# Kernel optimization log

Measured on AMD Instinct MI355X. Metric: run time of the kernel, lower is better.

## Reference

```python
import jax, jax.numpy as jnp
import numpy as np

BETA = 0.1
NUM_LAYERS = 2  # GT layers inside each FastGTN


def densify(edge_index, edge_weight, num_nodes):
    # edge_index: [T, 2, E] int, edge_weight: [T, E] -> dense [T, N, N]
    T, _, E = edge_index.shape
    t_ids = jnp.broadcast_to(jnp.arange(T)[:, None], (T, E))
    dense = jnp.zeros((T, num_nodes, num_nodes), dtype=edge_weight.dtype)
    return dense.at[t_ids, edge_index[:, 0, :], edge_index[:, 1, :]].add(edge_weight)


def fast_gtn(dense_A, X, Ws, conv_w, lin_w, lin_b, num_nodes):
    # Ws: [C, w_in, w_out]; conv_w: [L, C, T]; lin_w: [C*w_out, w_out]
    H = jnp.einsum('nk,ckh->cnh', X, Ws)              # [C, N, w_out]
    X_ = jax.lax.stop_gradient(H)                      # clone().detach()
    for l in range(NUM_LAYERS):
        filt = jax.nn.softmax(conv_w[l], axis=1)       # [C, T]
        adj = jnp.einsum('ct,tij->cij', filt, dense_A) # [C, N, N]
        H = jnp.einsum('cij,cjh->cih', adj, H)         # graph conv per channel
    H_ = jax.nn.relu(BETA * X_ + (1.0 - BETA) * H)     # [C, N, w_out]
    H_ = jnp.transpose(H_, (1, 0, 2)).reshape(num_nodes, -1)  # [N, C*w_out]
    return jax.nn.relu(H_ @ lin_w + lin_b)             # [N, w_out]


def setup_inputs() -> dict:
    key = jax.random.key(0)
    ks = jax.random.split(key, 12)
    T, E, N = 4, 131072, 4096
    C, F_IN, H_OUT = 2, 128, 64
    edge_index = jax.random.randint(ks[0], (T, 2, E), 0, N, dtype=jnp.int64)
    edge_weight = jax.random.uniform(ks[1], (T, E), dtype=jnp.float32)
    X = jax.random.normal(ks[2], (N, F_IN), dtype=jnp.float32)
    def glorot(k, shape):
        fan_in, fan_out = shape[-2], shape[-1]
        s = jnp.sqrt(6.0 / (fan_in + fan_out))
        return jax.random.uniform(k, shape, jnp.float32, -s, s)
    # FastGTN #1 (w_in=F_IN)
    Ws1 = glorot(ks[3], (C, F_IN, H_OUT))
    conv_w1 = 0.1 * jax.random.normal(ks[4], (NUM_LAYERS, C, T), dtype=jnp.float32)
    lin_w1 = glorot(ks[5], (C * H_OUT, H_OUT))
    lin_b1 = jnp.zeros((H_OUT,), jnp.float32)
    # FastGTN #2 (w_in=H_OUT)
    Ws2 = glorot(ks[6], (C, H_OUT, H_OUT))
    conv_w2 = 0.1 * jax.random.normal(ks[7], (NUM_LAYERS, C, T), dtype=jnp.float32)
    lin_w2 = glorot(ks[8], (C * H_OUT, H_OUT))
    lin_b2 = jnp.zeros((H_OUT,), jnp.float32)
    return {"edge_index": edge_index, "edge_weight": edge_weight, "X": X,
            "Ws1": Ws1, "conv_w1": conv_w1, "lin_w1": lin_w1, "lin_b1": lin_b1,
            "Ws2": Ws2, "conv_w2": conv_w2, "lin_w2": lin_w2, "lin_b2": lin_b2}


def reference(edge_index, edge_weight, X, Ws1, conv_w1, lin_w1, lin_b1,
              Ws2, conv_w2, lin_w2, lin_b2):
    N = X.shape[0]
    dense_A = densify(edge_index, edge_weight, N)      # [T, N, N]
    H = fast_gtn(dense_A, X, Ws1, conv_w1, lin_w1, lin_b1, N)
    H = fast_gtn(dense_A, H, Ws2, conv_w2, lin_w2, lin_b2, N)
    return H
```

## Files before the change

kernel.cpp:

```cpp
#include <hip/hip_runtime.h>

#define E_EDGES 131072
#define N_NODES 4096
#define HOUT    64
#define NE_TOT  (4 * E_EDGES)
#define CAP     256
#define CSTRIDE 16
#define SC_NBLK 64
#define SC_NTHR 1024
#define SC_EPB  (NE_TOT / SC_NBLK)
#define SC_EPT  (SC_EPB / SC_NTHR)

__device__ __forceinline__ unsigned short f2bf(float x) {
    unsigned u = __float_as_uint(x);
    return (unsigned short)((u + 0x7FFFu + ((u >> 16) & 1u)) >> 16);
}
__device__ __forceinline__ float bf2f(unsigned b) {
    return __uint_as_float(b << 16);
}

__device__ __forceinline__ void softmax4(const float* __restrict__ cw,
                                         int layer, int c, float f[4]) {
#pragma unroll
    for (int t = 0; t < 4; ++t) f[t] = cw[(layer * 2 + c) * 4 + t];
    float m = fmaxf(fmaxf(f[0], f[1]), fmaxf(f[2], f[3]));
    float s = 0.f;
#pragma unroll
    for (int t = 0; t < 4; ++t) { f[t] = expf(f[t] - m); s += f[t]; }
    float inv = 1.0f / s;
#pragma unroll
    for (int t = 0; t < 4; ++t) f[t] *= inv;
}

__device__ __forceinline__ float selw(const float f[4], int t) {
    float a = (t & 1) ? f[1] : f[0];
    float b = (t & 1) ? f[3] : f[2];
    return (t & 2) ? b : a;
}

__device__ __forceinline__ void fma8(float acc[8], float w, uint4 v) {
    acc[0] += w * bf2f(v.x & 0xFFFFu); acc[1] += w * bf2f(v.x >> 16);
    acc[2] += w * bf2f(v.y & 0xFFFFu); acc[3] += w * bf2f(v.y >> 16);
    acc[4] += w * bf2f(v.z & 0xFFFFu); acc[5] += w * bf2f(v.z >> 16);
    acc[6] += w * bf2f(v.w & 0xFFFFu); acc[7] += w * bf2f(v.w >> 16);
}

__device__ __forceinline__ uint4 pack8(const float acc[8]) {
    uint4 r;
    r.x = (unsigned)f2bf(acc[0]) | ((unsigned)f2bf(acc[1]) << 16);
    r.y = (unsigned)f2bf(acc[2]) | ((unsigned)f2bf(acc[3]) << 16);
    r.z = (unsigned)f2bf(acc[4]) | ((unsigned)f2bf(acc[5]) << 16);
    r.w = (unsigned)f2bf(acc[6]) | ((unsigned)f2bf(acc[7]) << 16);
    return r;
}

__device__ __forceinline__ void spmm_row2c(const unsigned* __restrict__ rowe, int len,
                                           const unsigned* __restrict__ Hc0,
                                           const unsigned* __restrict__ Hc1,
                                           const float f0[4], const float f1[4],
                                           int lane, float a0[8], float a1[8]) {
    int g  = lane >> 3;
    int hq = lane & 7;
#pragma unroll
    for (int j = 0; j < 8; ++j) { a0[j] = 0.f; a1[j] = 0.f; }
    int e = 0;
    for (; e + 16 <= len; e += 16) {
        unsigned r0 = rowe[e + g];
        unsigned r1 = rowe[e + 8 + g];
        int   d0 = r0 & 0xFFF, t0 = (r0 >> 12) & 3;
        int   d1 = r1 & 0xFFF, t1 = (r1 >> 12) & 3;
        float w0 = bf2f(r0 >> 16), w1 = bf2f(r1 >> 16);
        uint4 v00 = ((const uint4*)(Hc0 + d0 * (HOUT / 2)))[hq];
        uint4 v01 = ((const uint4*)(Hc1 + d0 * (HOUT / 2)))[hq];
        uint4 v10 = ((const uint4*)(Hc0 + d1 * (HOUT / 2)))[hq];
        uint4 v11 = ((const uint4*)(Hc1 + d1 * (HOUT / 2)))[hq];
        fma8(a0, w0 * selw(f0, t0), v00);
        fma8(a1, w0 * selw(f1, t0), v01);
        fma8(a0, w1 * selw(f0, t1), v10);
        fma8(a1, w1 * selw(f1, t1), v11);
    }
    for (; e + 8 <= len; e += 8) {
        unsigned r0 = rowe[e + g];
        int   d0 = r0 & 0xFFF, t0 = (r0 >> 12) & 3;
        float w0 = bf2f(r0 >> 16);
        uint4 v00 = ((const uint4*)(Hc0 + d0 * (HOUT / 2)))[hq];
        uint4 v01 = ((const uint4*)(Hc1 + d0 * (HOUT / 2)))[hq];
        fma8(a0, w0 * selw(f0, t0), v00);
        fma8(a1, w0 * selw(f1, t0), v01);
    }
    if (g < len - e) {
        unsigned r0 = rowe[e + g];
        int   d0 = r0 & 0xFFF, t0 = (r0 >> 12) & 3;
        float w0 = bf2f(r0 >> 16);
        uint4 v00 = ((const uint4*)(Hc0 + d0 * (HOUT / 2)))[hq];
        uint4 v01 = ((const uint4*)(Hc1 + d0 * (HOUT / 2)))[hq];
        fma8(a0, w0 * selw(f0, t0), v00);
        fma8(a1, w0 * selw(f1, t0), v01);
    }
#pragma unroll
    for (int j = 0; j < 8; ++j) {
        a0[j] += __shfl_xor(a0[j], 8);
        a0[j] += __shfl_xor(a0[j], 16);
        a0[j] += __shfl_xor(a0[j], 32);
        a1[j] += __shfl_xor(a1[j], 8);
        a1[j] += __shfl_xor(a1[j], 16);
        a1[j] += __shfl_xor(a1[j], 32);
    }
}

__global__ void __launch_bounds__(256)
zinit_kernel(const float* __restrict__ X, const float* __restrict__ Ws,
             float* __restrict__ H0, unsigned* __restrict__ H016,
             int* __restrict__ cursor) {
    int idx = blockIdx.x * 256 + threadIdx.x;
    if (idx < N_NODES * CSTRIDE) cursor[idx] = 0;
    int h = idx & 63;
    int n = (idx >> 6) & (N_NODES - 1);
    int c = idx >> 18;
    const float4* xv = (const float4*)(X + n * 128);
    const float*  w  = Ws + c * 128 * HOUT + h;
    float acc = 0.f;
#pragma unroll 8
    for (int k4 = 0; k4 < 32; ++k4) {
        float4 xx = xv[k4];
        acc += xx.x * w[(k4 * 4 + 0) * HOUT];
        acc += xx.y * w[(k4 * 4 + 1) * HOUT];
        acc += xx.z * w[(k4 * 4 + 2) * HOUT];
        acc += xx.w * w[(k4 * 4 + 3) * HOUT];
    }
    H0[idx] = acc;
    ((unsigned short*)H016)[idx] = f2bf(acc);
}

__global__ void __launch_bounds__(SC_NTHR)
scatter_kernel(const int* __restrict__ ei, const float* __restrict__ ew,
               int* __restrict__ gcursor, unsigned* __restrict__ edges) {
    __shared__ int shist[N_NODES];
    __shared__ int sbase[N_NODES];
    int tid = threadIdx.x;
    int t   = blockIdx.x >> 4;
    int e0  = (blockIdx.x & 15) * SC_EPB + tid * SC_EPT;
    const int*   ps = ei + (t * 2 + 0) * E_EDGES + e0;
    const int*   pd = ei + (t * 2 + 1) * E_EDGES + e0;
    const float* pw = ew + t * E_EDGES + e0;
#pragma unroll
    for (int j = 0; j < 4; ++j) shist[tid * 4 + j] = 0;
    __syncthreads();

    int4   s0 = ((const int4*)ps)[0],  s1 = ((const int4*)ps)[1];
    int4   d0 = ((const int4*)pd)[0],  d1 = ((const int4*)pd)[1];
    float4 w0 = ((const float4*)pw)[0], w1 = ((const float4*)pw)[1];
    int   srcs[8] = {s0.x, s0.y, s0.z, s0.w, s1.x, s1.y, s1.z, s1.w};
    int   dsts[8] = {d0.x, d0.y, d0.z, d0.w, d1.x, d1.y, d1.z, d1.w};
    float wts[8]  = {w0.x, w0.y, w0.z, w0.w, w1.x, w1.y, w1.z, w1.w};
    int lpos[8];
#pragma unroll
    for (int j = 0; j < 8; ++j) lpos[j] = atomicAdd(&shist[srcs[j]], 1);
    __syncthreads();

#pragma unroll
    for (int j = 0; j < 4; ++j) {
        int b = tid * 4 + j;
        int cntb = shist[b];
        if (cntb) sbase[b] = atomicAdd(&gcursor[b * CSTRIDE], cntb);
    }
    __syncthreads();

    unsigned tb = (unsigned)t << 12;
#pragma unroll
    for (int j = 0; j < 8; ++j) {
        unsigned p = (unsigned)(sbase[srcs[j]] + lpos[j]);
        unsigned rec = ((unsigned)f2bf(wts[j]) << 16) | tb | (unsigned)dsts[j];
        if (p < CAP) edges[srcs[j] * CAP + p] = rec;
    }
}

__global__ void __launch_bounds__(256)
spmm_kernel(const int* __restrict__ cnt, const unsigned* __restrict__ edges,
            const unsigned* __restrict__ Hin16, unsigned* __restrict__ Hout16,
            const float* __restrict__ cw) {
    int row  = (blockIdx.x * 256 + threadIdx.x) >> 6;
    int lane = threadIdx.x & 63;
    float f0[4], f1[4];
    softmax4(cw, 0, 0, f0);
    softmax4(cw, 0, 1, f1);
    int len = min(cnt[row * CSTRIDE], CAP);
    float a0[8], a1[8];
    spmm_row2c(edges + row * CAP, len,
               Hin16, Hin16 + N_NODES * (HOUT / 2), f0, f1, lane, a0, a1);
    if ((lane >> 3) == 0) {
        int hq = lane & 7;
        ((uint4*)(Hout16 + row * (HOUT / 2)))[hq] = pack8(a0);
        ((uint4*)(Hout16 + (N_NODES + row) * (HOUT / 2)))[hq] = pack8(a1);
    }
}

template <bool FINAL>
__global__ void __launch_bounds__(256)
tail_kernel(const int* __restrict__ cnt, const unsigned* __restrict__ edges,
            const unsigned* __restrict__ Hin16,
            const float* __restrict__ H0,
            const float* __restrict__ cw,
            const float* __restrict__ lw, const float* __restrict__ lb,
            const float* __restrict__ Wsn,
            float* __restrict__ outp, unsigned* __restrict__ out16) {
    __shared__ float hcomb[4][2 * HOUT];
    __shared__ float mids[4][HOUT];
    int tid  = threadIdx.x;
    int r    = tid >> 6;
    int lane = tid & 63;
    int row  = blockIdx.x * 4 + r;

    float f0[4], f1[4];
    softmax4(cw, 1, 0, f0);
    softmax4(cw, 1, 1, f1);
    int len = min(cnt[row * CSTRIDE], CAP);
    float a0[8], a1[8];
    spmm_row2c(edges + row * CAP, len,
               Hin16, Hin16 + N_NODES * (HOUT / 2), f0, f1, lane, a0, a1);

    if ((lane >> 3) == 0) {
        int hq = lane & 7;
#pragma unroll
        for (int j = 0; j < 8; ++j) {
            int h = hq * 8 + j;
            float h00 = H0[row * HOUT + h];
            float h01 = H0[(N_NODES + row) * HOUT + h];
            hcomb[r][h]        = fmaxf(0.1f * h00 + 0.9f * a0[j], 0.f);
            hcomb[r][HOUT + h] = fmaxf(0.1f * h01 + 0.9f * a1[j], 0.f);
        }
    }
    __syncthreads();

    float a = lb[lane];
#pragma unroll 8
    for (int j = 0; j < 2 * HOUT; ++j) a += hcomb[r][j] * lw[j * HOUT + lane];

    if (FINAL) {
        outp[row * HOUT + lane] = fmaxf(a, 0.f);
    } else {
        mids[r][lane] = fmaxf(a, 0.f);
        __syncthreads();
#pragma unroll
        for (int c = 0; c < 2; ++c) {
            float acc = 0.f;
            const float* w = Wsn + c * HOUT * HOUT + lane;
#pragma unroll 8
            for (int k = 0; k < HOUT; ++k) acc += mids[r][k] * w[k * HOUT];
            int o = (c * N_NODES + row) * HOUT + lane;
            outp[o] = acc;
            ((unsigned short*)out16)[o] = f2bf(acc);
        }
    }
}

extern "C" void kernel_launch(void* const* d_in, const int* in_sizes, int n_in,
                              void* d_out, int out_size, void* d_ws, size_t ws_size,
                              hipStream_t stream) {
    const int*   ei  = (const int*)d_in[0];
    const float* ew  = (const float*)d_in[1];
    const float* X   = (const float*)d_in[2];
    const float* Ws1 = (const float*)d_in[3];
    const float* cw1 = (const float*)d_in[4];
    const float* lw1 = (const float*)d_in[5];
    const float* lb1 = (const float*)d_in[6];
    const float* Ws2 = (const float*)d_in[7];
    const float* cw2 = (const float*)d_in[8];
    const float* lw2 = (const float*)d_in[9];
    const float* lb2 = (const float*)d_in[10];
    float* outp = (float*)d_out;

    char* ws = (char*)d_ws;
    size_t off = 0;
    auto alloc = [&](size_t bytes) -> void* {
        void* p = ws + off;
        off += (bytes + 255) & ~size_t(255);
        return p;
    };
    int*      cursor = (int*)alloc((size_t)N_NODES * CSTRIDE * 4);
    unsigned* edges  = (unsigned*)alloc((size_t)N_NODES * CAP * 4);
    float*    H0a    = (float*)alloc((size_t)2 * N_NODES * HOUT * 4);
    unsigned* H0a16  = (unsigned*)alloc((size_t)2 * N_NODES * HOUT * 2);
    unsigned* Ha16   = (unsigned*)alloc((size_t)2 * N_NODES * HOUT * 2);
    float*    H0b    = (float*)alloc((size_t)2 * N_NODES * HOUT * 4);
    unsigned* H0b16  = (unsigned*)alloc((size_t)2 * N_NODES * HOUT * 2);

    zinit_kernel  <<<2048, 256, 0, stream>>>(X, Ws1, H0a, H0a16, cursor);
    scatter_kernel<<<SC_NBLK, SC_NTHR, 0, stream>>>(ei, ew, cursor, edges);

    spmm_kernel<<<1024, 256, 0, stream>>>(cursor, edges, H0a16, Ha16, cw1);
    tail_kernel<false><<<1024, 256, 0, stream>>>(
        cursor, edges, Ha16, H0a, cw1, lw1, lb1, Ws2, H0b, H0b16);

    spmm_kernel<<<1024, 256, 0, stream>>>(cursor, edges, H0b16, Ha16, cw2);
    tail_kernel<true><<<1024, 256, 0, stream>>>(
        cursor, edges, Ha16, H0b, cw2, lw2, lb2, nullptr, outp, nullptr);
}
```

Measured before the change: 105.0 us.

## Interleave bf16 channel features per node and unroll SpMM edge loop to 32

Changes the bf16 feature buffer from channel-major to node-major, so a node's two channels sit in one contiguous 256-byte span. Each gathered neighbor then touches adjacent cache lines instead of two regions 512 KB apart. The SpMM main loop is also unrolled from 16 to 32 edges per iteration to keep more independent gathers in flight. The deeper unroll raises register pressure and sends more rows to the remainder loops.

```diff
diff --git a/kernel.cpp b/kernel.cpp
--- a/kernel.cpp
+++ b/kernel.cpp
@@ -55,8 +55,7 @@
 }
 
 __device__ __forceinline__ void spmm_row2c(const unsigned* __restrict__ rowe, int len,
-                                           const unsigned* __restrict__ Hc0,
-                                           const unsigned* __restrict__ Hc1,
+                                           const unsigned* __restrict__ H16,
                                            const float f0[4], const float f1[4],
                                            int lane, float a0[8], float a1[8]) {
     int g  = lane >> 3;
@@ -64,27 +63,40 @@
 #pragma unroll
     for (int j = 0; j < 8; ++j) { a0[j] = 0.f; a1[j] = 0.f; }
     int e = 0;
-    for (; e + 16 <= len; e += 16) {
+    for (; e + 32 <= len; e += 32) {
         unsigned r0 = rowe[e + g];
         unsigned r1 = rowe[e + 8 + g];
+        unsigned r2 = rowe[e + 16 + g];
+        unsigned r3 = rowe[e + 24 + g];
         int   d0 = r0 & 0xFFF, t0 = (r0 >> 12) & 3;
         int   d1 = r1 & 0xFFF, t1 = (r1 >> 12) & 3;
+        int   d2 = r2 & 0xFFF, t2 = (r2 >> 12) & 3;
+        int   d3 = r3 & 0xFFF, t3 = (r3 >> 12) & 3;
         float w0 = bf2f(r0 >> 16), w1 = bf2f(r1 >> 16);
-        uint4 v00 = ((const uint4*)(Hc0 + d0 * (HOUT / 2)))[hq];
-        uint4 v01 = ((const uint4*)(Hc1 + d0 * (HOUT / 2)))[hq];
-        uint4 v10 = ((const uint4*)(Hc0 + d1 * (HOUT / 2)))[hq];
-        uint4 v11 = ((const uint4*)(Hc1 + d1 * (HOUT / 2)))[hq];
+        float w2 = bf2f(r2 >> 16), w3 = bf2f(r3 >> 16);
+        uint4 v00 = ((const uint4*)(H16 + (d0 * 2 + 0) * 32))[hq];
+        uint4 v01 = ((const uint4*)(H16 + (d0 * 2 + 1) * 32))[hq];
+        uint4 v10 = ((const uint4*)(H16 + (d1 * 2 + 0) * 32))[hq];
+        uint4 v11 = ((const uint4*)(H16 + (d1 * 2 + 1) * 32))[hq];
+        uint4 v20 = ((const uint4*)(H16 + (d2 * 2 + 0) * 32))[hq];
+        uint4 v21 = ((const uint4*)(H16 + (d2 * 2 + 1) * 32))[hq];
+        uint4 v30 = ((const uint4*)(H16 + (d3 * 2 + 0) * 32))[hq];
+        uint4 v31 = ((const uint4*)(H16 + (d3 * 2 + 1) * 32))[hq];
         fma8(a0, w0 * selw(f0, t0), v00);
         fma8(a1, w0 * selw(f1, t0), v01);
         fma8(a0, w1 * selw(f0, t1), v10);
         fma8(a1, w1 * selw(f1, t1), v11);
+        fma8(a0, w2 * selw(f0, t2), v20);
+        fma8(a1, w2 * selw(f1, t2), v21);
+        fma8(a0, w3 * selw(f0, t3), v30);
+        fma8(a1, w3 * selw(f1, t3), v31);
     }
     for (; e + 8 <= len; e += 8) {
         unsigned r0 = rowe[e + g];
         int   d0 = r0 & 0xFFF, t0 = (r0 >> 12) & 3;
         float w0 = bf2f(r0 >> 16);
-        uint4 v00 = ((const uint4*)(Hc0 + d0 * (HOUT / 2)))[hq];
-        uint4 v01 = ((const uint4*)(Hc1 + d0 * (HOUT / 2)))[hq];
+        uint4 v00 = ((const uint4*)(H16 + (d0 * 2 + 0) * 32))[hq];
+        uint4 v01 = ((const uint4*)(H16 + (d0 * 2 + 1) * 32))[hq];
         fma8(a0, w0 * selw(f0, t0), v00);
         fma8(a1, w0 * selw(f1, t0), v01);
     }
@@ -92,8 +104,8 @@
         unsigned r0 = rowe[e + g];
         int   d0 = r0 & 0xFFF, t0 = (r0 >> 12) & 3;
         float w0 = bf2f(r0 >> 16);
-        uint4 v00 = ((const uint4*)(Hc0 + d0 * (HOUT / 2)))[hq];
-        uint4 v01 = ((const uint4*)(Hc1 + d0 * (HOUT / 2)))[hq];
+        uint4 v00 = ((const uint4*)(H16 + (d0 * 2 + 0) * 32))[hq];
+        uint4 v01 = ((const uint4*)(H16 + (d0 * 2 + 1) * 32))[hq];
         fma8(a0, w0 * selw(f0, t0), v00);
         fma8(a1, w0 * selw(f1, t0), v01);
     }
@@ -129,7 +141,7 @@
         acc += xx.w * w[(k4 * 4 + 3) * HOUT];
     }
     H0[idx] = acc;
-    ((unsigned short*)H016)[idx] = f2bf(acc);
+    ((unsigned short*)H016)[(n * 2 + c) * HOUT + h] = f2bf(acc);
 }
 
 __global__ void __launch_bounds__(SC_NTHR)
@@ -186,12 +198,11 @@
     softmax4(cw, 0, 1, f1);
     int len = min(cnt[row * CSTRIDE], CAP);
     float a0[8], a1[8];
-    spmm_row2c(edges + row * CAP, len,
-               Hin16, Hin16 + N_NODES * (HOUT / 2), f0, f1, lane, a0, a1);
+    spmm_row2c(edges + row * CAP, len, Hin16, f0, f1, lane, a0, a1);
     if ((lane >> 3) == 0) {
         int hq = lane & 7;
-        ((uint4*)(Hout16 + row * (HOUT / 2)))[hq] = pack8(a0);
-        ((uint4*)(Hout16 + (N_NODES + row) * (HOUT / 2)))[hq] = pack8(a1);
+        ((uint4*)(Hout16 + (row * 2 + 0) * 32))[hq] = pack8(a0);
+        ((uint4*)(Hout16 + (row * 2 + 1) * 32))[hq] = pack8(a1);
     }
 }
 
@@ -216,8 +227,7 @@
     softmax4(cw, 1, 1, f1);
     int len = min(cnt[row * CSTRIDE], CAP);
     float a0[8], a1[8];
-    spmm_row2c(edges + row * CAP, len,
-               Hin16, Hin16 + N_NODES * (HOUT / 2), f0, f1, lane, a0, a1);
+    spmm_row2c(edges + row * CAP, len, Hin16, f0, f1, lane, a0, a1);
 
     if ((lane >> 3) == 0) {
         int hq = lane & 7;
@@ -247,9 +257,8 @@
             const float* w = Wsn + c * HOUT * HOUT + lane;
 #pragma unroll 8
             for (int k = 0; k < HOUT; ++k) acc += mids[r][k] * w[k * HOUT];
-            int o = (c * N_NODES + row) * HOUT + lane;
-            outp[o] = acc;
-            ((unsigned short*)out16)[o] = f2bf(acc);
+            outp[(c * N_NODES + row) * HOUT + lane] = acc;
+            ((unsigned short*)out16)[(row * 2 + c) * HOUT + lane] = f2bf(acc);
         }
     }
 }
```

After: 102.1 us. 1.03x faster.
